# Optimization experiments

Hardware: AMD Instinct MI355X
Metric: run time of the kernel (lower is better)

The kernel has to match this reference:

```python
import jax, jax.numpy as jnp
import numpy as np
from jax import lax


def setup_inputs() -> dict:
    key = jax.random.key(0)
    ks = jax.random.split(key, 10)
    B, M, C, H, W, D = 4, 4, 32, 32, 32, 32
    R = 8  # rank = dim // rank_ratio
    inp = {
        "x_aligned": jax.random.normal(ks[0], (B, M, C, H, W, D), jnp.float32),
        "spatial_basis": 0.02 * jax.random.normal(ks[1], (1, R, H, W, D), jnp.float32),
        "mixer_w": 0.02 * jax.random.normal(ks[2], (C, R), jnp.float32),
        "wq": 0.02 * jax.random.normal(ks[3], (M + 1, C, C), jnp.float32),
        "wk": 0.02 * jax.random.normal(ks[4], (M + 1, C, C), jnp.float32),
        "wv": 0.02 * jax.random.normal(ks[5], (M + 1, C, C), jnp.float32),
        "conv1_w": 0.02 * jax.random.normal(ks[6], (2 * C, M * C, 5, 5, 5), jnp.float32),
        "conv1_b": 0.02 * jax.random.normal(ks[7], (2 * C,), jnp.float32),
        "conv2_w": 0.02 * jax.random.normal(ks[8], (C, 2 * C, 5, 5, 5), jnp.float32),
        "conv2_b": 0.02 * jax.random.normal(ks[9], (C,), jnp.float32),
        # torch init is alpha=0; use 0.5 so the attention branch contributes
        "alpha": jnp.full((1,), 0.5, jnp.float32),
    }
    return inp


DN = ("NCHWD", "OIHWD", "NCHWD")  # 3D conv dim numbers
PAD = [(2, 2), (2, 2), (2, 2)]    # k=5, d=1 -> p=2 (same)


def reference(x_aligned, spatial_basis, mixer_w, wq, wk, wv,
              conv1_w, conv1_b, conv2_w, conv2_b, alpha):
    B, M, C, H, W, D = x_aligned.shape
    # fused token: 1x1 conv mixing rank -> dim, broadcast over batch
    token = jnp.einsum('or,rhwd->ohwd', mixer_w, spatial_basis[0])       # [C,H,W,D]
    token = jnp.broadcast_to(token[None, None], (B, 1, C, H, W, D))
    x_all = jnp.concatenate([x_aligned, token], axis=1)                  # [B,M+1,C,H,W,D]
    # grouped 1x1 conv QKV == per-group channel matmul
    q = jnp.einsum('goc,bgchwd->bgohwd', wq, x_all)
    k = jnp.einsum('goc,bgchwd->bgohwd', wk, x_all)
    v = jnp.einsum('goc,bgchwd->bgohwd', wv, x_all)
    scale = C ** (-0.5)
    attn = jnp.einsum('bichwd,bjchwd->bijhwd', q, k) * scale             # [B,5,5,H,W,D]
    attn = jax.nn.softmax(attn, axis=2)
    out = jnp.einsum('bijhwd,bjchwd->bichwd', attn, v)
    att_fused = out[:, -1]                                               # [B,C,H,W,D]
    # parallel conv branch
    conv_in = x_aligned.reshape(B, M * C, H, W, D)
    h = lax.conv_general_dilated(conv_in, conv1_w, (1, 1, 1), PAD,
                                 dimension_numbers=DN)
    h = h + conv1_b[None, :, None, None, None]
    h = jax.nn.gelu(h, approximate=False)
    cnn = lax.conv_general_dilated(h, conv2_w, (1, 1, 1), PAD,
                                   dimension_numbers=DN)
    cnn = cnn + conv2_b[None, :, None, None, None]
    return cnn + alpha[0] * att_fused
```

## Files before the change

### kernel.cpp

```cpp
#include <hip/hip_runtime.h>
#include <cstddef>
#include <cstdint>

#define S3 32768

typedef short bf16x8 __attribute__((ext_vector_type(8)));
typedef float f32x16 __attribute__((ext_vector_type(16)));

static __device__ inline unsigned short f2bf(float f) {
    unsigned int u = __float_as_uint(f);
    unsigned int r = (u + 0x7FFFu + ((u >> 16) & 1u)) >> 16;
    return (unsigned short)r;
}

static __device__ inline float bf2f(unsigned short u) {
    return __uint_as_float(((unsigned)u) << 16);
}

template <int IC, int OC>
__global__ __launch_bounds__(256) void wt_transpose(
    const float* __restrict__ w, unsigned short* __restrict__ wT)
{
    constexpr int ICB = IC / 32, WOC = OC / 32;
    constexpr int NFLAT = IC * 125;
    constexpr int NRUNS = 125 * ICB * 4;
    __shared__ unsigned short tile[IC][130];
    const int oc = blockIdx.x, tid = threadIdx.x;
    const int ln = oc & 31, c = oc >> 5;
    const float* src = w + (size_t)oc * NFLAT;

    for (int f = tid; f < NFLAT / 4; f += 256) {
        float4 v = *(const float4*)(src + f * 4);
        float vv[4] = {v.x, v.y, v.z, v.w};
#pragma unroll
        for (int i = 0; i < 4; ++i) {
            int flat = f * 4 + i;
            int ic = flat / 125, tap = flat - ic * 125;
            tile[ic][tap] = f2bf(vv[i]);
        }
    }
    __syncthreads();
    for (int r = tid; r < NRUNS; r += 256) {
        int tap = r / (ICB * 4);
        int rem = r - tap * (ICB * 4);
        int icb = rem >> 2, kb = (rem >> 1) & 1, half = rem & 1;
        int ic0 = icb * 32 + kb * 16 + half * 8;
        __align__(16) unsigned short tmp[8];
#pragma unroll
        for (int e = 0; e < 8; ++e) tmp[e] = tile[ic0 + e][tap];
        size_t t = ((((size_t)(tap * ICB + icb) * WOC + c) * 2 + kb) * 64 +
                    half * 32 + ln) * 8;
        *(uint4*)(wT + t) = *(const uint4*)tmp;
    }
}

__global__ __launch_bounds__(256) void xb_transpose(
    const float* __restrict__ x, unsigned short* __restrict__ xb)
{
    __shared__ float tile[32][133];
    int zy = blockIdx.x, b = blockIdx.y;
    int t = threadIdx.x, xi = t & 31, ich = t >> 5;
#pragma unroll
    for (int k = 0; k < 16; ++k) {
        int ic = k * 8 + ich;
        tile[xi][ic] = x[(size_t)(b * 128 + ic) * S3 + zy * 32 + xi];
    }
    __syncthreads();
#pragma unroll
    for (int k = 0; k < 2; ++k) {
        int u = t + 256 * k;
        int xx = u >> 4, j = u & 15;
        __align__(16) unsigned short tmp[8];
#pragma unroll
        for (int e = 0; e < 8; ++e) tmp[e] = f2bf(tile[xx][j * 8 + e]);
        *(uint4*)(xb + ((size_t)b * S3 + zy * 32 + xx) * 128 + j * 8) =
            *(const uint4*)tmp;
    }
}

__global__ __launch_bounds__(256) void attention_mfma(
    const unsigned short* __restrict__ xb, const float* __restrict__ basis,
    const float* __restrict__ mixer, const float* __restrict__ wq,
    const float* __restrict__ wk, const float* __restrict__ wv,
    const float* __restrict__ alpha_p, float* __restrict__ out)
{
    const int wave = threadIdx.x >> 6, lane = threadIdx.x & 63;
    const int ln = lane & 31, half = lane >> 5;
    const int tl = blockIdx.x * 4 + wave;
    const int g0 = tl * 32;
    const int b = g0 >> 15;
    const int s0 = g0 & (S3 - 1);

    bf16x8 aq[2], ak[5][2], av[5][2];
#pragma unroll
    for (int kb = 0; kb < 2; ++kb) {
        const float* qs = wq + 4 * 1024 + ln * 32 + kb * 16 + half * 8;
        bf16x8 tq;
#pragma unroll
        for (int e = 0; e < 8; ++e) tq[e] = (short)f2bf(qs[e]);
        aq[kb] = tq;
    }
#pragma unroll
    for (int j = 0; j < 5; ++j)
#pragma unroll
        for (int kb = 0; kb < 2; ++kb) {
            const float* ks = wk + ((j * 32 + ln) * 32 + kb * 16 + half * 8);
            const float* vs = wv + ((j * 32 + ln) * 32 + kb * 16 + half * 8);
            bf16x8 tk, tv;
#pragma unroll
            for (int e = 0; e < 8; ++e) {
                tk[e] = (short)f2bf(ks[e]);
                tv[e] = (short)f2bf(vs[e]);
            }
            ak[j][kb] = tk;
            av[j][kb] = tv;
        }

    float bv[8];
#pragma unroll
    for (int r = 0; r < 8; ++r) bv[r] = basis[r * S3 + s0 + ln];
    bf16x8 tokf[2];
#pragma unroll
    for (int kb = 0; kb < 2; ++kb) {
        bf16x8 tf;
#pragma unroll
        for (int e = 0; e < 8; ++e) {
            int c = kb * 16 + half * 8 + e;
            float t = 0.f;
#pragma unroll
            for (int r = 0; r < 8; ++r) t += mixer[c * 8 + r] * bv[r];
            tf[e] = (short)f2bf(t);
        }
        tokf[kb] = tf;
    }

    f32x16 qc;
#pragma unroll
    for (int e = 0; e < 16; ++e) qc[e] = 0.f;
    qc = __builtin_amdgcn_mfma_f32_32x32x16_bf16(aq[0], tokf[0], qc, 0, 0, 0);
    qc = __builtin_amdgcn_mfma_f32_32x32x16_bf16(aq[1], tokf[1], qc, 0, 0, 0);

    const unsigned short* xrow = xb + ((size_t)b * S3 + s0 + ln) * 128;

    auto loadB = [&](int j, int kb) -> bf16x8 {
        if (j < 4)
            return *(const bf16x8*)(xrow + j * 32 + kb * 16 + half * 8);
        else
            return tokf[kb];
    };

    const float scale = 0.17677669529663687f;
    float l[5];
#pragma unroll
    for (int j = 0; j < 5; ++j) {
        bf16x8 b0 = loadB(j, 0), b1 = loadB(j, 1);
        f32x16 c;
#pragma unroll
        for (int e = 0; e < 16; ++e) c[e] = 0.f;
        c = __builtin_amdgcn_mfma_f32_32x32x16_bf16(ak[j][0], b0, c, 0, 0, 0);
        c = __builtin_amdgcn_mfma_f32_32x32x16_bf16(ak[j][1], b1, c, 0, 0, 0);
        float part = 0.f;
#pragma unroll
        for (int r = 0; r < 16; ++r) part += c[r] * qc[r];
        part += __shfl_xor(part, 32);
        l[j] = part * scale;
    }

    float m = l[0];
#pragma unroll
    for (int j = 1; j < 5; ++j) m = fmaxf(m, l[j]);
    float p[5], sum = 0.f;
#pragma unroll
    for (int j = 0; j < 5; ++j) { p[j] = __expf(l[j] - m); sum += p[j]; }
    float inv = alpha_p[0] / sum;

    f32x16 ov;
#pragma unroll
    for (int e = 0; e < 16; ++e) ov[e] = 0.f;
#pragma unroll
    for (int j = 0; j < 5; ++j) {
        float pj = p[j];
#pragma unroll
        for (int kb = 0; kb < 2; ++kb) {
            bf16x8 bx = loadB(j, kb);
            bf16x8 pb;
#pragma unroll
            for (int e = 0; e < 8; ++e)
                pb[e] = (short)f2bf(bf2f((unsigned short)bx[e]) * pj);
            ov = __builtin_amdgcn_mfma_f32_32x32x16_bf16(av[j][kb], pb, ov,
                                                         0, 0, 0);
        }
    }

#pragma unroll
    for (int r = 0; r < 16; ++r) {
        int row = (r & 3) + 8 * (r >> 2) + 4 * half;
        out[((size_t)b * 32 + row) * S3 + s0 + ln] = ov[r] * inv;
    }
}

template <int IC, int OC, bool WRITE_H>
__global__ __launch_bounds__(512, 2) void conv_mfma(
    const unsigned short* __restrict__ xin, const uint4* __restrict__ wTq,
    const float* __restrict__ bias, unsigned short* __restrict__ hout,
    float* __restrict__ fout)
{
    constexpr int ICB = IC / 32, WOC = OC / 32;
    constexpr int JT = 2 * WOC;
    constexpr int NW = ICB * 5;
    constexpr int NIN = 2880;
    constexpr int BUF = 20 * 36 * 80;
    __shared__ __align__(16) char lds_in[2 * BUF];

    const int tid = threadIdx.x;
    const int wave = tid >> 6, lane = tid & 63;
    const int ln = lane & 31, half = lane >> 5;
    const int ochalf = (WOC == 2) ? (wave >> 2) : 0;
    const int wy = (WOC == 2) ? (wave & 3) : wave;
    const int z = blockIdx.x, ybl = blockIdx.y, b = blockIdx.z;
    const int y0 = ybl * 16;

    const uint4* wTl = wTq + half * 32 + ln;

    int  goff[6];
    int  loff[6];
    bool act[6], yxok[6];
#pragma unroll
    for (int k = 0; k < 6; ++k) {
        int i = tid + 512 * k;
        act[k] = i < NIN;
        int sub = i & 3, cc = i >> 2;
        int x36 = cc % 36, row = cc / 36;
        int gy = y0 - 2 + row, gx = x36 - 2;
        yxok[k] = ((unsigned)gy < 32u) & ((unsigned)gx < 32u);
        goff[k] = (b * 32768 + gy * 32 + gx) * IC + sub * 8;
        loff[k] = row * 2880 + x36 * 80 + sub * 16;
    }

    f32x16 acc[JT];
#pragma unroll
    for (int j = 0; j < JT; ++j)
#pragma unroll
        for (int e = 0; e < 16; ++e) acc[j][e] = 0.f;

    uint4 prei[6];

    auto issue = [&](int icb, int dz) {
        int gz = z + dz - 2;
        bool zok = (unsigned)gz < 32u;
        int zoff = gz * (1024 * IC) + icb * 32;
#pragma unroll
        for (int k = 0; k < 6; ++k) {
            if (act[k]) {
                uint4 v = {0u, 0u, 0u, 0u};
                if (zok & yxok[k])
                    v = *(const uint4*)(xin + goff[k] + zoff);
                prei[k] = v;
            }
        }
    };

    auto stage = [&](int buf) {
        char* base = lds_in + buf * BUF;
#pragma unroll
        for (int k = 0; k < 6; ++k)
            if (act[k]) *(uint4*)(base + loff[k]) = prei[k];
    };

    bf16x8 bufA[5], bufB[5];

    auto fillA = [&](bool valid, int icb, int dz, int dx, int kb,
                     bf16x8 (&buf)[5]) {
        if (!valid) return;
#pragma unroll
        for (int dy = 0; dy < 5; ++dy) {
            int tap = (dz * 5 + dy) * 5 + dx;
            int f = ((tap * ICB + icb) * WOC + ochalf) * 2 + kb;
            buf[dy] = *(const bf16x8*)(wTl + (size_t)f * 64);
        }
    };

    auto compute = [&](const char* base, bf16x8 (&cur)[5], int dx, int kb) {
        bf16x8 brow[JT + 4];
#pragma unroll
        for (int r = 0; r < JT + 4; ++r)
            brow[r] = *(const bf16x8*)(base + (JT * wy + r) * 2880 +
                                       (ln + dx) * 80 + kb * 32 + half * 16);
#pragma unroll
        for (int dy = 0; dy < 5; ++dy)
#pragma unroll
            for (int j = 0; j < JT; ++j)
                acc[j] = __builtin_amdgcn_mfma_f32_32x32x16_bf16(
                    cur[dy], brow[dy + j], acc[j], 0, 0, 0);
    };

    issue(0, 0);
    fillA(true, 0, 0, 0, 0, bufA);
    stage(0);
    __syncthreads();

    int cur = 0;
    for (int w = 0; w < NW; ++w) {
        int icb = w / 5, dz = w - icb * 5;
        int nw = w + 1;
        int nicb = nw / 5, ndz = nw - nicb * 5;
        bool more = nw < NW;
        const char* rb = lds_in + cur * BUF;

#pragma unroll
        for (int gp = 0; gp < 5; ++gp) {
            fillA(true, icb, dz, gp, 1, bufB);
            compute(rb, bufA, gp, 0);
            if (gp < 4) fillA(true, icb, dz, gp + 1, 0, bufA);
            else        fillA(more, nicb, ndz, 0, 0, bufA);
            if (gp == 0 && more) issue(nicb, ndz);
            if (gp == 2 && more) stage(cur ^ 1);
            compute(rb, bufB, gp, 1);
        }
        asm volatile("s_waitcnt lgkmcnt(0)\n\ts_barrier" ::: "memory");
        cur ^= 1;
    }

    __syncthreads();
    if (WRITE_H) {
#pragma unroll
        for (int j = 0; j < JT; ++j) {
            char* scr = lds_in + wy * (32 * 144);
#pragma unroll
            for (int r = 0; r < 16; ++r) {
                int ocr = (r & 3) + 8 * (r >> 2) + 4 * half;
                int oc = ochalf * 32 + ocr;
                float v = acc[j][r] + bias[oc];
                v = 0.5f * v * (1.f + erff(v * 0.70710678118654752f));
                *(unsigned short*)(scr + ln * 144 + oc * 2) = f2bf(v);
            }
            __syncthreads();
#pragma unroll
            for (int k = 0; k < 2; ++k) {
                int u = tid + 512 * k;
                int wyi = u >> 8, rem = u & 255;
                int xx = rem >> 3, un = rem & 7;
                uint4 v = *(const uint4*)(lds_in + wyi * (32 * 144) +
                                          xx * 144 + un * 16);
                int y = y0 + 4 * wyi + j;
                *(uint4*)(hout + ((((size_t)b * 32 + z) * 32 + y) * 32 + xx)
                          * 64 + un * 8) = v;
            }
            __syncthreads();
        }
    } else {
#pragma unroll
        for (int j = 0; j < JT; ++j) {
            int y = y0 + JT * wy + j;
#pragma unroll
            for (int r = 0; r < 16; ++r) {
                int oc = (r & 3) + 8 * (r >> 2) + 4 * half;
                size_t o = ((size_t)b * 32 + oc) * S3 + z * 1024 + y * 32 + ln;
                fout[o] = acc[j][r] + bias[oc] + fout[o];
            }
        }
    }
}

template <int IC, int OC, bool WRITE_H>
__global__ __launch_bounds__(512, 2) void conv_mfma_ks(
    const unsigned short* __restrict__ xin, const uint4* __restrict__ wTq,
    const float* __restrict__ bias, unsigned short* __restrict__ hout,
    float* __restrict__ fout)
{
    constexpr int ICB = IC / 32, WOC = OC / 32;
    constexpr int JT = (WOC == 2) ? 8 : 4;
    constexpr int NW = ICB * 5;
    constexpr int NIN = 2880;
    constexpr int BUF = 20 * 36 * 80;
    constexpr int PREI = 6;
    __shared__ __align__(16) char lds_in[2 * BUF];

    const int tid = threadIdx.x;
    const int wave = tid >> 6, lane = tid & 63;
    const int ln = lane & 31, half = lane >> 5;
    const int kbw = wave & 1;
    const int w2 = wave >> 1;
    const int ochalf = (WOC == 2) ? (w2 >> 1) : 0;
    const int wy = (WOC == 2) ? (w2 & 1) : w2;
    const int z = blockIdx.x, ybl = blockIdx.y, b = blockIdx.z;
    const int y0 = ybl * 16;

    const uint4* wTl = wTq + half * 32 + ln;

    int  goff[PREI];
    bool act[PREI], yxok[PREI];
#pragma unroll
    for (int k = 0; k < PREI; ++k) {
        int i = tid + 512 * k;
        act[k] = i < NIN;
        int sub = i & 3, cc = i >> 2;
        int x36 = cc % 36, row = cc / 36;
        int gy = y0 - 2 + row, gx = x36 - 2;
        yxok[k] = ((unsigned)gy < 32u) & ((unsigned)gx < 32u);
        goff[k] = (b * 32768 + gy * 32 + gx) * IC + sub * 8;
    }

    f32x16 acc[JT];
#pragma unroll
    for (int j = 0; j < JT; ++j)
#pragma unroll
        for (int e = 0; e < 16; ++e) acc[j][e] = 0.f;

    uint4 prei[PREI];

    auto issue = [&](int icb, int dz) {
        int gz = z + dz - 2;
        bool zok = (unsigned)gz < 32u;
        int zoff = gz * (1024 * IC) + icb * 32;
#pragma unroll
        for (int k = 0; k < PREI; ++k) {
            if (act[k]) {
                uint4 v = {0u, 0u, 0u, 0u};
                if (zok & yxok[k])
                    v = *(const uint4*)(xin + goff[k] + zoff);
                prei[k] = v;
            }
        }
    };

    auto stage = [&](int buf) {
        char* base = lds_in + buf * BUF;
#pragma unroll
        for (int k = 0; k < PREI; ++k) {
            if (act[k]) {
                int i = tid + 512 * k;
                int sub = i & 3, cc = i >> 2;
                int row = cc / 36, x36 = cc - row * 36;
                *(uint4*)(base + row * 2880 + x36 * 80 + sub * 16) = prei[k];
            }
        }
    };

    bf16x8 bufA[5], bufB[5];

    auto fillA = [&](bool valid, int icb, int dz, int dx, bf16x8 (&buf)[5]) {
        if (!valid) return;
#pragma unroll
        for (int dy = 0; dy < 5; ++dy) {
            int tap = (dz * 5 + dy) * 5 + dx;
            int f = ((tap * ICB + icb) * WOC + ochalf) * 2 + kbw;
            buf[dy] = *(const bf16x8*)(wTl + (size_t)f * 64);
        }
    };

    auto compute = [&](const char* base, bf16x8 (&cur)[5], int dx) {
        bf16x8 brow[JT + 4];
#pragma unroll
        for (int r = 0; r < JT + 4; ++r)
            brow[r] = *(const bf16x8*)(base + (JT * wy + r) * 2880 +
                                       (ln + dx) * 80 + kbw * 32 + half * 16);
#pragma unroll
        for (int dy = 0; dy < 5; ++dy)
#pragma unroll
            for (int j = 0; j < JT; ++j)
                acc[j] = __builtin_amdgcn_mfma_f32_32x32x16_bf16(
                    cur[dy], brow[dy + j], acc[j], 0, 0, 0);
    };

    int cur = 0;
    auto window = [&](int w, bf16x8 (&X)[5], bf16x8 (&Y)[5]) {
        int icb = w / 5, dz = w - icb * 5;
        int nw = w + 1;
        int nicb = nw / 5, ndz = nw - nicb * 5;
        bool more = nw < NW;
        const char* rb = lds_in + cur * BUF;

        fillA(true, icb, dz, 1, Y);
        if (more) issue(nicb, ndz);
        compute(rb, X, 0);
        fillA(true, icb, dz, 2, X);
        compute(rb, Y, 1);
        fillA(true, icb, dz, 3, Y);
        if (more) stage(cur ^ 1);
        compute(rb, X, 2);
        fillA(true, icb, dz, 4, X);
        compute(rb, Y, 3);
        fillA(more, nicb, ndz, 0, Y);
        compute(rb, X, 4);
        asm volatile("s_waitcnt lgkmcnt(0)\n\ts_barrier" ::: "memory");
        cur ^= 1;
    };

    issue(0, 0);
    fillA(true, 0, 0, 0, bufA);
    stage(0);
    __syncthreads();

    for (int wp = 0; wp < NW; wp += 2) {
        window(wp, bufA, bufB);
        window(wp + 1, bufB, bufA);
    }

    __syncthreads();
    {
        char* red = lds_in;
#pragma unroll
        for (int rnd = 0; rnd < JT / 4; ++rnd) {
            if (kbw == 1) {
#pragma unroll
                for (int qi = 0; qi < 4; ++qi) {
                    const uint4* src = (const uint4*)&acc[rnd * 4 + qi];
#pragma unroll
                    for (int wd = 0; wd < 4; ++wd)
                        *(uint4*)(red + (w2 * 4 + qi) * 5120 + lane * 80 +
                                  wd * 16) = src[wd];
                }
            }
            __syncthreads();
            if (kbw == 0) {
#pragma unroll
                for (int qi = 0; qi < 4; ++qi) {
#pragma unroll
                    for (int wd = 0; wd < 4; ++wd) {
                        uint4 v = *(const uint4*)(red + (w2 * 4 + qi) * 5120 +
                                                  lane * 80 + wd * 16);
                        acc[rnd * 4 + qi][wd * 4 + 0] += __uint_as_float(v.x);
                        acc[rnd * 4 + qi][wd * 4 + 1] += __uint_as_float(v.y);
                        acc[rnd * 4 + qi][wd * 4 + 2] += __uint_as_float(v.z);
                        acc[rnd * 4 + qi][wd * 4 + 3] += __uint_as_float(v.w);
                    }
                }
            }
            __syncthreads();
        }
    }

    if (WRITE_H) {
#pragma unroll
        for (int j = 0; j < JT; ++j) {
            if (kbw == 0) {
                char* scr = lds_in + wy * (32 * 144);
#pragma unroll
                for (int r = 0; r < 16; ++r) {
                    int ocr = (r & 3) + 8 * (r >> 2) + 4 * half;
                    int oc = ochalf * 32 + ocr;
                    float v = acc[j][r] + bias[oc];
                    v = 0.5f * v * (1.f + erff(v * 0.70710678118654752f));
                    *(unsigned short*)(scr + ln * 144 + oc * 2) = f2bf(v);
                }
            }
            __syncthreads();
            {
                int u = tid;
                int wyi = u >> 8, rem = u & 255;
                int xx = rem >> 3, un = rem & 7;
                uint4 v = *(const uint4*)(lds_in + wyi * (32 * 144) +
                                          xx * 144 + un * 16);
                int y = y0 + 8 * wyi + j;
                *(uint4*)(hout + ((((size_t)b * 32 + z) * 32 + y) * 32 + xx)
                          * 64 + un * 8) = v;
            }
            __syncthreads();
        }
    } else {
        if (kbw == 0) {
#pragma unroll
            for (int j = 0; j < JT; ++j) {
                int y = y0 + JT * wy + j;
#pragma unroll
                for (int r = 0; r < 16; ++r) {
                    int oc = (r & 3) + 8 * (r >> 2) + 4 * half;
                    size_t o = ((size_t)b * 32 + oc) * S3 + z * 1024 + y * 32 + ln;
                    fout[o] = acc[j][r] + bias[oc] + fout[o];
                }
            }
        }
    }
}

extern "C" void kernel_launch(void* const* d_in, const int* in_sizes, int n_in,
                              void* d_out, int out_size, void* d_ws, size_t ws_size,
                              hipStream_t stream)
{
    const float* x       = (const float*)d_in[0];
    const float* basis   = (const float*)d_in[1];
    const float* mixer   = (const float*)d_in[2];
    const float* wq      = (const float*)d_in[3];
    const float* wk      = (const float*)d_in[4];
    const float* wv      = (const float*)d_in[5];
    const float* conv1_w = (const float*)d_in[6];
    const float* conv1_b = (const float*)d_in[7];
    const float* conv2_w = (const float*)d_in[8];
    const float* conv2_b = (const float*)d_in[9];
    const float* alpha   = (const float*)d_in[10];
    float* out = (float*)d_out;

    char* wsb = (char*)d_ws;
    unsigned short* xb   = (unsigned short*)wsb;
    unsigned short* h    = (unsigned short*)(wsb + 33554432);
    unsigned short* wT1  = (unsigned short*)(wsb + 50331648);
    unsigned short* wT2  = (unsigned short*)(wsb + 52379648);

    wt_transpose<128, 64><<<64, 256, 0, stream>>>(conv1_w, wT1);
    wt_transpose<64, 32><<<32, 256, 0, stream>>>(conv2_w, wT2);
    xb_transpose<<<dim3(1024, 4), 256, 0, stream>>>(x, xb);

    attention_mfma<<<1024, 256, 0, stream>>>(xb, basis, mixer, wq, wk, wv,
                                             alpha, out);

    conv_mfma<128, 64, true><<<dim3(32, 2, 4), 512, 0, stream>>>(
        xb, (const uint4*)wT1, conv1_b, h, nullptr);
    conv_mfma_ks<64, 32, false><<<dim3(32, 2, 4), 512, 0, stream>>>(
        h, (const uint4*)wT2, conv2_b, nullptr, out);
}
```

Before: 442.4 us.

## Fuse token attention into conv2 epilogue via LDS staging

Removes the separate attention kernel and computes the per-voxel attention inside the conv2 kernel's epilogue. Results go into LDS and are added directly with bias, so the output is no longer written by one kernel and then read back and rewritten by another. This saves a launch and a full read-modify-write of the output tensor. In exchange the conv2 kernel gets longer, with extra register pressure and MFMA work on only 256 blocks, and QKV weights are reloaded and converted from global memory in every block.

Result: slower. 468.7 us (+5.9%).

```diff
diff --git a/kernel.cpp b/kernel.cpp
--- a/kernel.cpp
+++ b/kernel.cpp
@@ -75,127 +75,6 @@
         for (int e = 0; e < 8; ++e) tmp[e] = f2bf(tile[xx][j * 8 + e]);
         *(uint4*)(xb + ((size_t)b * S3 + zy * 32 + xx) * 128 + j * 8) =
             *(const uint4*)tmp;
-    }
-}
-
-__global__ __launch_bounds__(256) void attention_mfma(
-    const unsigned short* __restrict__ xb, const float* __restrict__ basis,
-    const float* __restrict__ mixer, const float* __restrict__ wq,
-    const float* __restrict__ wk, const float* __restrict__ wv,
-    const float* __restrict__ alpha_p, float* __restrict__ out)
-{
-    const int wave = threadIdx.x >> 6, lane = threadIdx.x & 63;
-    const int ln = lane & 31, half = lane >> 5;
-    const int tl = blockIdx.x * 4 + wave;
-    const int g0 = tl * 32;
-    const int b = g0 >> 15;
-    const int s0 = g0 & (S3 - 1);
-
-    bf16x8 aq[2], ak[5][2], av[5][2];
-#pragma unroll
-    for (int kb = 0; kb < 2; ++kb) {
-        const float* qs = wq + 4 * 1024 + ln * 32 + kb * 16 + half * 8;
-        bf16x8 tq;
-#pragma unroll
-        for (int e = 0; e < 8; ++e) tq[e] = (short)f2bf(qs[e]);
-        aq[kb] = tq;
-    }
-#pragma unroll
-    for (int j = 0; j < 5; ++j)
-#pragma unroll
-        for (int kb = 0; kb < 2; ++kb) {
-            const float* ks = wk + ((j * 32 + ln) * 32 + kb * 16 + half * 8);
-            const float* vs = wv + ((j * 32 + ln) * 32 + kb * 16 + half * 8);
-            bf16x8 tk, tv;
-#pragma unroll
-            for (int e = 0; e < 8; ++e) {
-                tk[e] = (short)f2bf(ks[e]);
-                tv[e] = (short)f2bf(vs[e]);
-            }
-            ak[j][kb] = tk;
-            av[j][kb] = tv;
-        }
-
-    float bv[8];
-#pragma unroll
-    for (int r = 0; r < 8; ++r) bv[r] = basis[r * S3 + s0 + ln];
-    bf16x8 tokf[2];
-#pragma unroll
-    for (int kb = 0; kb < 2; ++kb) {
-        bf16x8 tf;
-#pragma unroll
-        for (int e = 0; e < 8; ++e) {
-            int c = kb * 16 + half * 8 + e;
-            float t = 0.f;
-#pragma unroll
-            for (int r = 0; r < 8; ++r) t += mixer[c * 8 + r] * bv[r];
-            tf[e] = (short)f2bf(t);
-        }
-        tokf[kb] = tf;
-    }
-
-    f32x16 qc;
-#pragma unroll
-    for (int e = 0; e < 16; ++e) qc[e] = 0.f;
-    qc = __builtin_amdgcn_mfma_f32_32x32x16_bf16(aq[0], tokf[0], qc, 0, 0, 0);
-    qc = __builtin_amdgcn_mfma_f32_32x32x16_bf16(aq[1], tokf[1], qc, 0, 0, 0);
-
-    const unsigned short* xrow = xb + ((size_t)b * S3 + s0 + ln) * 128;
-
-    auto loadB = [&](int j, int kb) -> bf16x8 {
-        if (j < 4)
-            return *(const bf16x8*)(xrow + j * 32 + kb * 16 + half * 8);
-        else
-            return tokf[kb];
-    };
-
-    const float scale = 0.17677669529663687f;
-    float l[5];
-#pragma unroll
-    for (int j = 0; j < 5; ++j) {
-        bf16x8 b0 = loadB(j, 0), b1 = loadB(j, 1);
-        f32x16 c;
-#pragma unroll
-        for (int e = 0; e < 16; ++e) c[e] = 0.f;
-        c = __builtin_amdgcn_mfma_f32_32x32x16_bf16(ak[j][0], b0, c, 0, 0, 0);
-        c = __builtin_amdgcn_mfma_f32_32x32x16_bf16(ak[j][1], b1, c, 0, 0, 0);
-        float part = 0.f;
-#pragma unroll
-        for (int r = 0; r < 16; ++r) part += c[r] * qc[r];
-        part += __shfl_xor(part, 32);
-        l[j] = part * scale;
-    }
-
-    float m = l[0];
-#pragma unroll
-    for (int j = 1; j < 5; ++j) m = fmaxf(m, l[j]);
-    float p[5], sum = 0.f;
-#pragma unroll
-    for (int j = 0; j < 5; ++j) { p[j] = __expf(l[j] - m); sum += p[j]; }
-    float inv = alpha_p[0] / sum;
-
-    f32x16 ov;
-#pragma unroll
-    for (int e = 0; e < 16; ++e) ov[e] = 0.f;
-#pragma unroll
-    for (int j = 0; j < 5; ++j) {
-        float pj = p[j];
-#pragma unroll
-        for (int kb = 0; kb < 2; ++kb) {
-            bf16x8 bx = loadB(j, kb);
-            bf16x8 pb;
-#pragma unroll
-            for (int e = 0; e < 8; ++e)
-                pb[e] = (short)f2bf(bf2f((unsigned short)bx[e]) * pj);
-            ov = __builtin_amdgcn_mfma_f32_32x32x16_bf16(av[j][kb], pb, ov,
-                                                         0, 0, 0);
-        }
-    }
-
-#pragma unroll
-    for (int r = 0; r < 16; ++r) {
-        int row = (r & 3) + 8 * (r >> 2) + 4 * half;
-        out[((size_t)b * 32 + row) * S3 + s0 + ln] = ov[r] * inv;
     }
 }
 
@@ -366,7 +245,11 @@
 __global__ __launch_bounds__(512, 2) void conv_mfma_ks(
     const unsigned short* __restrict__ xin, const uint4* __restrict__ wTq,
     const float* __restrict__ bias, unsigned short* __restrict__ hout,
-    float* __restrict__ fout)
+    float* __restrict__ fout,
+    const unsigned short* __restrict__ xb, const float* __restrict__ basis,
+    const float* __restrict__ mixer, const float* __restrict__ wq,
+    const float* __restrict__ wk, const float* __restrict__ wv,
+    const float* __restrict__ alpha_p)
 {
     constexpr int ICB = IC / 32, WOC = OC / 32;
     constexpr int JT = (WOC == 2) ? 8 : 4;
@@ -559,15 +442,120 @@
             __syncthreads();
         }
     } else {
+        float* att = (float*)lds_in;
+        const float alpha = alpha_p[0];
+        const float scale = 0.17677669529663687f;
+#pragma unroll
+        for (int rr = 0; rr < 2; ++rr) {
+            int rb = wave * 2 + rr;
+            int s0 = z * 1024 + (y0 + rb) * 32;
+
+            float bvv[8];
+#pragma unroll
+            for (int r = 0; r < 8; ++r) bvv[r] = basis[r * S3 + s0 + ln];
+            bf16x8 tokf[2];
+#pragma unroll
+            for (int kb = 0; kb < 2; ++kb) {
+                bf16x8 tf;
+#pragma unroll
+                for (int e = 0; e < 8; ++e) {
+                    int c = kb * 16 + half * 8 + e;
+                    float t = 0.f;
+#pragma unroll
+                    for (int r = 0; r < 8; ++r) t += mixer[c * 8 + r] * bvv[r];
+                    tf[e] = (short)f2bf(t);
+                }
+                tokf[kb] = tf;
+            }
+
+            auto wfrag = [&](const float* wsrc) -> bf16x8 {
+                bf16x8 tw;
+#pragma unroll
+                for (int e = 0; e < 8; ++e) tw[e] = (short)f2bf(wsrc[e]);
+                return tw;
+            };
+
+            f32x16 qc;
+#pragma unroll
+            for (int e = 0; e < 16; ++e) qc[e] = 0.f;
+#pragma unroll
+            for (int kb = 0; kb < 2; ++kb)
+                qc = __builtin_amdgcn_mfma_f32_32x32x16_bf16(
+                    wfrag(wq + 4 * 1024 + ln * 32 + kb * 16 + half * 8),
+                    tokf[kb], qc, 0, 0, 0);
+
+            const unsigned short* xrow =
+                xb + ((size_t)b * S3 + s0 + ln) * 128;
+            auto loadB = [&](int j, int kb) -> bf16x8 {
+                if (j < 4)
+                    return *(const bf16x8*)(xrow + j * 32 + kb * 16 +
+                                            half * 8);
+                return tokf[kb];
+            };
+
+            float l[5];
+#pragma unroll
+            for (int j = 0; j < 5; ++j) {
+                f32x16 c;
+#pragma unroll
+                for (int e = 0; e < 16; ++e) c[e] = 0.f;
+#pragma unroll
+                for (int kb = 0; kb < 2; ++kb)
+                    c = __builtin_amdgcn_mfma_f32_32x32x16_bf16(
+                        wfrag(wk + (j * 32 + ln) * 32 + kb * 16 + half * 8),
+                        loadB(j, kb), c, 0, 0, 0);
+                float part = 0.f;
+#pragma unroll
+                for (int r = 0; r < 16; ++r) part += c[r] * qc[r];
+                part += __shfl_xor(part, 32);
+                l[j] = part * scale;
+            }
+
+            float mx = l[0];
+#pragma unroll
+            for (int j = 1; j < 5; ++j) mx = fmaxf(mx, l[j]);
+            float p[5], sum = 0.f;
+#pragma unroll
+            for (int j = 0; j < 5; ++j) { p[j] = __expf(l[j] - mx); sum += p[j]; }
+            float inv = alpha / sum;
+
+            f32x16 ov;
+#pragma unroll
+            for (int e = 0; e < 16; ++e) ov[e] = 0.f;
+#pragma unroll
+            for (int j = 0; j < 5; ++j) {
+                float pj = p[j];
+#pragma unroll
+                for (int kb = 0; kb < 2; ++kb) {
+                    bf16x8 bx = loadB(j, kb);
+                    bf16x8 pb;
+#pragma unroll
+                    for (int e = 0; e < 8; ++e)
+                        pb[e] = (short)f2bf(bf2f((unsigned short)bx[e]) * pj);
+                    ov = __builtin_amdgcn_mfma_f32_32x32x16_bf16(
+                        wfrag(wv + (j * 32 + ln) * 32 + kb * 16 + half * 8),
+                        pb, ov, 0, 0, 0);
+                }
+            }
+
+#pragma unroll
+            for (int r = 0; r < 16; ++r)
+                att[((rb * 2 + half) * 16 + r) * 32 + ln] = ov[r] * inv;
+        }
+        __syncthreads();
+
         if (kbw == 0) {
 #pragma unroll
             for (int j = 0; j < JT; ++j) {
-                int y = y0 + JT * wy + j;
+                int rb = 4 * wy + j;
+                int y = y0 + rb;
 #pragma unroll
                 for (int r = 0; r < 16; ++r) {
                     int oc = (r & 3) + 8 * (r >> 2) + 4 * half;
-                    size_t o = ((size_t)b * 32 + oc) * S3 + z * 1024 + y * 32 + ln;
-                    fout[o] = acc[j][r] + bias[oc] + fout[o];
+                    size_t o = ((size_t)b * 32 + oc) * S3 + z * 1024 +
+                               y * 32 + ln;
+                    fout[o] = acc[j][r] + bias[oc] +
+                              att[((rb * 2 + half) * 16 + r) * 32 + ln];
                 }
             }
         }
@@ -601,11 +589,9 @@
     wt_transpose<64, 32><<<32, 256, 0, stream>>>(conv2_w, wT2);
     xb_transpose<<<dim3(1024, 4), 256, 0, stream>>>(x, xb);
 
-    attention_mfma<<<1024, 256, 0, stream>>>(xb, basis, mixer, wq, wk, wv,
-                                             alpha, out);
-
     conv_mfma<128, 64, true><<<dim3(32, 2, 4), 512, 0, stream>>>(
         xb, (const uint4*)wT1, conv1_b, h, nullptr);
     conv_mfma_ks<64, 32, false><<<dim3(32, 2, 4), 512, 0, stream>>>(
-        h, (const uint4*)wT2, conv2_b, nullptr, out);
-}
+        h, (const uint4*)wT2, conv2_b, nullptr, out,
+        xb, basis, mixer, wq, wk, wv, alpha);
+}
```
